# Kernel optimization log

Measured on AMD Instinct MI355X. Metric: run time of the kernel, lower is better.

The kernel has to match this reference:

```python
import jax, jax.numpy as jnp
import numpy as np

NUM_EMBEDDINGS = 8192
EMBEDDING_DIM = 64
COMMITMENT_COST = 0.25


def setup_inputs() -> dict:
    key = jax.random.key(0)
    kx, ke = jax.random.split(key)
    x = jax.random.normal(kx, (32, 1024, EMBEDDING_DIM), dtype=jnp.float32)
    embeddings = jax.random.normal(ke, (NUM_EMBEDDINGS, EMBEDDING_DIM), dtype=jnp.float32)
    return {"x": x, "embeddings": embeddings}


def reference(x, embeddings):
    d = embeddings.shape[1]
    flat_x = x.reshape(-1, d)  # [N, D]
    # squared euclidean distances (argmin identical to cdist argmin):
    d2 = (
        jnp.sum(flat_x * flat_x, axis=-1, keepdims=True)
        - 2.0 * flat_x @ embeddings.T
        + jnp.sum(embeddings * embeddings, axis=-1)
    )
    encoding_indices = jnp.argmin(d2, axis=1)  # [N]
    quantized = embeddings[encoding_indices].reshape(x.shape)
    codebook_loss = jnp.mean((jax.lax.stop_gradient(quantized) - x) ** 2)
    commitment_loss = COMMITMENT_COST * jnp.mean((quantized - jax.lax.stop_gradient(x)) ** 2)
    loss = codebook_loss + commitment_loss
    # straight-through estimator
    quantized_st = x + jax.lax.stop_gradient(quantized - x)
    return quantized_st, loss, encoding_indices
```

## Files before the change

kernel.cpp:

```cpp
#include <hip/hip_runtime.h>
#include <hip/hip_bf16.h>
#include <float.h>

#define N_ROWS 32768
#define DIMS   64
#define K_EMB  8192
#define NT     (K_EMB / 16)
#define NTH    (NT / 2)
#define TSTAGE 8
#define NSTAGE (NTH / TSTAGE)
#define GAP_THR 1.5e-3f

typedef __attribute__((ext_vector_type(8))) short s8v;
typedef __attribute__((ext_vector_type(4))) float f4v;
typedef __attribute__((ext_vector_type(4))) int   i4v;

#define WS_EFRAG 0
#define WS_EN2   (2 * 1024 * 1024)
#define WS_IDX   (WS_EN2 + K_EMB * 4)
#define WS_KEY   (WS_IDX + N_ROWS * 4)
#define WS_BH    (WS_KEY + N_ROWS * 8)
#define WS_SH    (WS_BH + 2 * N_ROWS * 4)
#define WS_CH    (WS_SH + 2 * N_ROWS * 4)
#define WS_CTL   (WS_CH + 2 * N_ROWS * 4)
#define WS_WL    (WS_CTL + 16)

#define OUT_LOSS (N_ROWS * DIMS)
#define OUT_IDX  (N_ROWS * DIMS + 1)

__device__ inline short bfh(float v) {
    __hip_bfloat16 h = __float2bfloat16(v);
    return __builtin_bit_cast(short, h);
}
__device__ inline float bff(short s) {
    __hip_bfloat16 h = __builtin_bit_cast(__hip_bfloat16, s);
    return __bfloat162float(h);
}

__global__ void vq_prep(const float* __restrict__ emb, short* __restrict__ efrag,
                        float* __restrict__ en2) {
    int gid = blockIdx.x * 256 + threadIdx.x;
    int t = gid >> 6, lane = gid & 63;
    int m = lane & 15, q = lane >> 4;
    const float* er = emb + (size_t)(t * 16 + m) * DIMS;
    s8v hi0, lo0, hi1, lo1;
    float ss = 0.f;
#pragma unroll
    for (int j = 0; j < 8; ++j) {
        float v0 = er[q * 8 + j];
        float v1 = er[32 + q * 8 + j];
        ss += v0 * v0 + v1 * v1;
        short h0 = bfh(v0); lo0[j] = bfh(v0 - bff(h0)); hi0[j] = h0;
        short h1 = bfh(v1); lo1[j] = bfh(v1 - bff(h1)); hi1[j] = h1;
    }
    s8v* base = (s8v*)efrag + (size_t)t * 4 * 64;
    base[0 * 64 + lane] = hi0;
    base[1 * 64 + lane] = hi1;
    base[2 * 64 + lane] = lo0;
    base[3 * 64 + lane] = lo1;
    ss += __shfl_xor(ss, 16, 64);
    ss += __shfl_xor(ss, 32, 64);
    if (q == 0) en2[t * 16 + m] = -0.5f * ss;
}

__global__ __launch_bounds__(256, 2) void vq_phase1(
    const float* __restrict__ x, const short* __restrict__ efrag,
    const float* __restrict__ en2,
    float* __restrict__ bh, float* __restrict__ sh, int* __restrict__ ch) {
    __shared__ __align__(16) char lds[2][TSTAGE * 4096];
    int tid = threadIdx.x, wid = tid >> 6, lane = tid & 63;
    int m = lane & 15, q = lane >> 4;
    int kh = blockIdx.y;
    int row0 = blockIdx.x * 128 + wid * 32;

    s8v ahi[2][2], alo[2][2];
#pragma unroll
    for (int g = 0; g < 2; ++g) {
        const float* xr = x + (size_t)(row0 + g * 16 + m) * DIMS + q * 8;
#pragma unroll
        for (int j = 0; j < 8; ++j) {
            float v0 = xr[j], v1 = xr[32 + j];
            short h0 = bfh(v0); alo[g][0][j] = bfh(v0 - bff(h0)); ahi[g][0][j] = h0;
            short h1 = bfh(v1); alo[g][1][j] = bfh(v1 - bff(h1)); ahi[g][1][j] = h1;
        }
    }

    float best[2][4], sec[2][4];
    int bc[2][4];
#pragma unroll
    for (int g = 0; g < 2; ++g)
#pragma unroll
        for (int r = 0; r < 4; ++r) { best[g][r] = -FLT_MAX; sec[g][r] = -FLT_MAX; bc[g][r] = 0; }

    const char* gsrc = (const char*)efrag + (size_t)kh * NTH * 4096;

#pragma unroll
    for (int i = 0; i < 8; ++i)
        __builtin_amdgcn_global_load_lds(
            (const __attribute__((address_space(1))) void*)(gsrc + i * 4096 + tid * 16),
            (__attribute__((address_space(3))) void*)(&lds[0][i * 4096 + tid * 16]),
            16, 0, 0);
    __syncthreads();

    for (int s = 0; s < NSTAGE; ++s) {
        int pb = s & 1;
        if (s + 1 < NSTAGE) {
            const char* gn = gsrc + (size_t)(s + 1) * TSTAGE * 4096;
#pragma unroll
            for (int i = 0; i < 8; ++i)
                __builtin_amdgcn_global_load_lds(
                    (const __attribute__((address_space(1))) void*)(gn + i * 4096 + tid * 16),
                    (__attribute__((address_space(3))) void*)(&lds[pb ^ 1][i * 4096 + tid * 16]),
                    16, 0, 0);
        }
        const i4v* B = (const i4v*)(lds[pb]);
        int tg0 = kh * NTH + s * TSTAGE;
        const float* ep = en2 + (size_t)tg0 * 16 + m;
#pragma unroll
        for (int tt = 0; tt < TSTAGE; ++tt) {
            i4v b0 = B[tt * 256 + 0 * 64 + lane];
            i4v b1 = B[tt * 256 + 1 * 64 + lane];
            i4v b2 = B[tt * 256 + 2 * 64 + lane];
            i4v b3 = B[tt * 256 + 3 * 64 + lane];
            float c0 = ep[tt * 16];
            int cidx = (tg0 + tt) * 16 + m;
#pragma unroll
            for (int g = 0; g < 2; ++g) {
                f4v acc = {c0, c0, c0, c0};
                acc = __builtin_amdgcn_mfma_f32_16x16x32_bf16(ahi[g][0], __builtin_bit_cast(s8v, b0), acc, 0, 0, 0);
                acc = __builtin_amdgcn_mfma_f32_16x16x32_bf16(ahi[g][1], __builtin_bit_cast(s8v, b1), acc, 0, 0, 0);
                acc = __builtin_amdgcn_mfma_f32_16x16x32_bf16(ahi[g][0], __builtin_bit_cast(s8v, b2), acc, 0, 0, 0);
                acc = __builtin_amdgcn_mfma_f32_16x16x32_bf16(ahi[g][1], __builtin_bit_cast(s8v, b3), acc, 0, 0, 0);
                acc = __builtin_amdgcn_mfma_f32_16x16x32_bf16(alo[g][0], __builtin_bit_cast(s8v, b0), acc, 0, 0, 0);
                acc = __builtin_amdgcn_mfma_f32_16x16x32_bf16(alo[g][1], __builtin_bit_cast(s8v, b1), acc, 0, 0, 0);
#pragma unroll
                for (int r = 0; r < 4; ++r) {
                    float v = acc[r];
                    bool gt = v > best[g][r];
                    sec[g][r]  = fmaxf(sec[g][r], fminf(v, best[g][r]));
                    best[g][r] = fmaxf(best[g][r], v);
                    bc[g][r]   = gt ? cidx : bc[g][r];
                }
            }
        }
        __syncthreads();
    }

#pragma unroll
    for (int g = 0; g < 2; ++g)
#pragma unroll
    for (int r = 0; r < 4; ++r) {
        float b = best[g][r], s = sec[g][r];
        int c = bc[g][r];
#pragma unroll
        for (int off = 1; off < 16; off <<= 1) {
            float ob = __shfl_xor(b, off, 64);
            float os = __shfl_xor(s, off, 64);
            int   oc = __shfl_xor(c, off, 64);
            float nb = fmaxf(b, ob);
            float ns = fmaxf(fminf(b, ob), fmaxf(s, os));
            bool take = (ob > b) || (ob == b && oc < c);
            c = take ? oc : c;
            b = nb; s = ns;
        }
        if (m == 0) {
            int o = kh * N_ROWS + row0 + g * 16 + q * 4 + r;
            bh[o] = b; sh[o] = s; ch[o] = c;
        }
    }
}

__global__ void vq_merge(const float* __restrict__ bh, const float* __restrict__ sh,
                         const int* __restrict__ ch, int* __restrict__ idx_buf,
                         unsigned long long* __restrict__ key8,
                         int* __restrict__ wl, int* __restrict__ wl_count) {
    int row = blockIdx.x * 256 + threadIdx.x;
    float b0 = bh[row], b1 = bh[N_ROWS + row];
    float s0 = sh[row], s1 = sh[N_ROWS + row];
    int   c0 = ch[row], c1 = ch[N_ROWS + row];
    float nb = fmaxf(b0, b1);
    float ns = fmaxf(fminf(b0, b1), fmaxf(s0, s1));
    int c = (b1 > b0) ? c1 : c0;
    idx_buf[row] = c;
    key8[row] = 0ULL;
    if (nb - ns < GAP_THR) {
        int pos = atomicAdd(wl_count, 1);
        wl[pos] = row;
    }
}

__global__ __launch_bounds__(256) void vq_fixup(
    const float* __restrict__ x, const float* __restrict__ emb,
    const float* __restrict__ en2, unsigned long long* __restrict__ key8,
    const int* __restrict__ wl, const int* __restrict__ wl_count) {
    __shared__ float4 sx[16];
    __shared__ float sbf[4];
    __shared__ int   sbc[4];
    int tid = threadIdx.x, wid = tid >> 6, lane = tid & 63;
    int cnt = *wl_count;
    for (int wi = blockIdx.x; wi < cnt * 8; wi += gridDim.x) {
        int row = wl[wi >> 3];
        int cbase = (wi & 7) * (K_EMB / 8);
        if (tid < 16) sx[tid] = ((const float4*)(x + (size_t)row * DIMS))[tid];
        __syncthreads();
        float bf_ = -FLT_MAX;
        int bc_ = 0;
        for (int c = cbase + tid; c < cbase + K_EMB / 8; c += 256) {
            const float4* er = (const float4*)(emb + (size_t)c * DIMS);
            float d = 0.f;
#pragma unroll
            for (int qq = 0; qq < 16; ++qq) {
                float4 e = er[qq];
                float4 xx = sx[qq];
                d += e.x * xx.x + e.y * xx.y + e.z * xx.z + e.w * xx.w;
            }
            float f = d + en2[c];
            if (f > bf_) { bf_ = f; bc_ = c; }
        }
#pragma unroll
        for (int off = 1; off < 64; off <<= 1) {
            float of = __shfl_xor(bf_, off, 64);
            int   oc = __shfl_xor(bc_, off, 64);
            if (of > bf_ || (of == bf_ && oc < bc_)) { bf_ = of; bc_ = oc; }
        }
        if (lane == 0) { sbf[wid] = bf_; sbc[wid] = bc_; }
        __syncthreads();
        if (tid == 0) {
            float b = sbf[0]; int c = sbc[0];
#pragma unroll
            for (int i = 1; i < 4; ++i)
                if (sbf[i] > b || (sbf[i] == b && sbc[i] < c)) { b = sbf[i]; c = sbc[i]; }
            unsigned int u = __float_as_uint(b);
            unsigned int sb = ((int)u < 0) ? ~u : (u | 0x80000000u);
            unsigned long long key = ((unsigned long long)sb << 32) | (unsigned int)(~c);
            atomicMax(&key8[row], key);
        }
        __syncthreads();
    }
}

__global__ void vq_gather(const float* __restrict__ x, const float* __restrict__ emb,
                          const int* __restrict__ idx_buf,
                          const unsigned long long* __restrict__ key8,
                          float* __restrict__ out, double* __restrict__ loss_acc) {
    int row = blockIdx.x * blockDim.x + threadIdx.x;
    unsigned long long k = key8[row];
    int idx = k ? (int)(~(unsigned int)k) : idx_buf[row];
    const float4* ev = (const float4*)(emb + (size_t)idx * DIMS);
    const float4* xv = (const float4*)(x + (size_t)row * DIMS);
    float4* ov = (float4*)(out + (size_t)row * DIMS);
    float s = 0.f;
#pragma unroll
    for (int qq = 0; qq < 16; ++qq) {
        float4 ee = ev[qq];
        float4 xx = xv[qq];
        float dx = ee.x - xx.x, dy = ee.y - xx.y, dz = ee.z - xx.z, dw = ee.w - xx.w;
        s += dx * dx + dy * dy + dz * dz + dw * dw;
        ov[qq] = ee;
    }
#pragma unroll
    for (int off = 32; off > 0; off >>= 1) s += __shfl_down(s, off, 64);
    if ((threadIdx.x & 63) == 0) atomicAdd(loss_acc, (double)s);
    out[OUT_IDX + row] = (float)idx;
}

__global__ void vq_loss(const double* __restrict__ acc, float* __restrict__ out) {
    out[OUT_LOSS] = (float)(1.25 * (*acc) / (double)(N_ROWS * DIMS));
}

extern "C" void kernel_launch(void* const* d_in, const int* in_sizes, int n_in,
                              void* d_out, int out_size, void* d_ws, size_t ws_size,
                              hipStream_t stream) {
    const float* x   = (const float*)d_in[0];
    const float* emb = (const float*)d_in[1];
    float* out = (float*)d_out;
    char*  ws  = (char*)d_ws;

    short* efrag   = (short*)(ws + WS_EFRAG);
    float* en2     = (float*)(ws + WS_EN2);
    int*   idx_buf = (int*)(ws + WS_IDX);
    unsigned long long* key8 = (unsigned long long*)(ws + WS_KEY);
    float* bhb     = (float*)(ws + WS_BH);
    float* shb     = (float*)(ws + WS_SH);
    int*   chb     = (int*)(ws + WS_CH);
    double* loss_acc = (double*)(ws + WS_CTL);
    int*   wl_count  = (int*)(ws + WS_CTL + 8);
    int*   wl        = (int*)(ws + WS_WL);

    hipMemsetAsync(ws + WS_CTL, 0, 16, stream);

    vq_prep<<<(NT * 64) / 256, 256, 0, stream>>>(emb, efrag, en2);
    vq_phase1<<<dim3(N_ROWS / 128, 2), 256, 0, stream>>>(x, efrag, en2, bhb, shb, chb);
    vq_merge<<<N_ROWS / 256, 256, 0, stream>>>(bhb, shb, chb, idx_buf, key8, wl, wl_count);
    vq_fixup<<<2048, 256, 0, stream>>>(x, emb, en2, key8, wl, wl_count);
    vq_gather<<<N_ROWS / 256, 256, 0, stream>>>(x, emb, idx_buf, key8, out, loss_acc);
    vq_loss<<<1, 1, 0, stream>>>(loss_acc, out);
}
```

Baseline: 199.6 us.

## Split codebook search into quarters, raise occupancy, restructure fixup as codebook-stationary

```diff
diff --git a/kernel.cpp b/kernel.cpp
--- a/kernel.cpp
+++ b/kernel.cpp
@@ -6,9 +6,10 @@
 #define DIMS   64
 #define K_EMB  8192
 #define NT     (K_EMB / 16)
-#define NTH    (NT / 2)
-#define TSTAGE 8
-#define NSTAGE (NTH / TSTAGE)
+#define NQ     4
+#define NTQ    (NT / NQ)
+#define TSTAGE 4
+#define NSTAGE (NTQ / TSTAGE)
 #define GAP_THR 1.5e-3f
 
 typedef __attribute__((ext_vector_type(8))) short s8v;
@@ -20,9 +21,9 @@
 #define WS_IDX   (WS_EN2 + K_EMB * 4)
 #define WS_KEY   (WS_IDX + N_ROWS * 4)
 #define WS_BH    (WS_KEY + N_ROWS * 8)
-#define WS_SH    (WS_BH + 2 * N_ROWS * 4)
-#define WS_CH    (WS_SH + 2 * N_ROWS * 4)
-#define WS_CTL   (WS_CH + 2 * N_ROWS * 4)
+#define WS_SH    (WS_BH + 4 * N_ROWS * 4)
+#define WS_CH    (WS_SH + 4 * N_ROWS * 4)
+#define WS_CTL   (WS_CH + 4 * N_ROWS * 4)
 #define WS_WL    (WS_CTL + 16)
 
 #define OUT_LOSS (N_ROWS * DIMS)
@@ -63,7 +64,7 @@
     if (q == 0) en2[t * 16 + m] = -0.5f * ss;
 }
 
-__global__ __launch_bounds__(256, 2) void vq_phase1(
+__global__ __launch_bounds__(256, 5) void vq_phase1(
     const float* __restrict__ x, const short* __restrict__ efrag,
     const float* __restrict__ en2,
     float* __restrict__ bh, float* __restrict__ sh, int* __restrict__ ch) {
@@ -92,10 +93,10 @@
 #pragma unroll
         for (int r = 0; r < 4; ++r) { best[g][r] = -FLT_MAX; sec[g][r] = -FLT_MAX; bc[g][r] = 0; }
 
-    const char* gsrc = (const char*)efrag + (size_t)kh * NTH * 4096;
-
-#pragma unroll
-    for (int i = 0; i < 8; ++i)
+    const char* gsrc = (const char*)efrag + (size_t)kh * NTQ * 4096;
+
+#pragma unroll
+    for (int i = 0; i < TSTAGE; ++i)
         __builtin_amdgcn_global_load_lds(
             (const __attribute__((address_space(1))) void*)(gsrc + i * 4096 + tid * 16),
             (__attribute__((address_space(3))) void*)(&lds[0][i * 4096 + tid * 16]),
@@ -107,14 +108,14 @@
         if (s + 1 < NSTAGE) {
             const char* gn = gsrc + (size_t)(s + 1) * TSTAGE * 4096;
 #pragma unroll
-            for (int i = 0; i < 8; ++i)
+            for (int i = 0; i < TSTAGE; ++i)
                 __builtin_amdgcn_global_load_lds(
                     (const __attribute__((address_space(1))) void*)(gn + i * 4096 + tid * 16),
                     (__attribute__((address_space(3))) void*)(&lds[pb ^ 1][i * 4096 + tid * 16]),
                     16, 0, 0);
         }
         const i4v* B = (const i4v*)(lds[pb]);
-        int tg0 = kh * NTH + s * TSTAGE;
+        int tg0 = kh * NTQ + s * TSTAGE;
         const float* ep = en2 + (size_t)tg0 * 16 + m;
 #pragma unroll
         for (int tt = 0; tt < TSTAGE; ++tt) {
@@ -137,7 +138,7 @@
                 for (int r = 0; r < 4; ++r) {
                     float v = acc[r];
                     bool gt = v > best[g][r];
-                    sec[g][r]  = fmaxf(sec[g][r], fminf(v, best[g][r]));
+                    sec[g][r]  = __builtin_amdgcn_fmed3f(v, sec[g][r], best[g][r]);
                     best[g][r] = fmaxf(best[g][r], v);
                     bc[g][r]   = gt ? cidx : bc[g][r];
                 }
@@ -173,69 +174,69 @@
 __global__ void vq_merge(const float* __restrict__ bh, const float* __restrict__ sh,
                          const int* __restrict__ ch, int* __restrict__ idx_buf,
                          unsigned long long* __restrict__ key8,
+                         float* __restrict__ nbv,
                          int* __restrict__ wl, int* __restrict__ wl_count) {
     int row = blockIdx.x * 256 + threadIdx.x;
-    float b0 = bh[row], b1 = bh[N_ROWS + row];
-    float s0 = sh[row], s1 = sh[N_ROWS + row];
-    int   c0 = ch[row], c1 = ch[N_ROWS + row];
-    float nb = fmaxf(b0, b1);
-    float ns = fmaxf(fminf(b0, b1), fmaxf(s0, s1));
-    int c = (b1 > b0) ? c1 : c0;
+    float nb = bh[row];
+    int   c  = ch[row];
+    float ns = -FLT_MAX;
+#pragma unroll
+    for (int h = 1; h < NQ; ++h) {
+        float b = bh[h * N_ROWS + row];
+        int   cc = ch[h * N_ROWS + row];
+        if (b > nb) { ns = nb; nb = b; c = cc; }
+        else        { ns = fmaxf(ns, b); }
+    }
+#pragma unroll
+    for (int h = 0; h < NQ; ++h) ns = fmaxf(ns, sh[h * N_ROWS + row]);
     idx_buf[row] = c;
     key8[row] = 0ULL;
+    nbv[row] = nb;
     if (nb - ns < GAP_THR) {
         int pos = atomicAdd(wl_count, 1);
         wl[pos] = row;
     }
 }
 
-__global__ __launch_bounds__(256) void vq_fixup(
+__global__ __launch_bounds__(64) void vq_fixup(
     const float* __restrict__ x, const float* __restrict__ emb,
-    const float* __restrict__ en2, unsigned long long* __restrict__ key8,
+    const float* __restrict__ en2, const float* __restrict__ nbv,
+    unsigned long long* __restrict__ key8,
     const int* __restrict__ wl, const int* __restrict__ wl_count) {
-    __shared__ float4 sx[16];
-    __shared__ float sbf[4];
-    __shared__ int   sbc[4];
-    int tid = threadIdx.x, wid = tid >> 6, lane = tid & 63;
+    int lane = threadIdx.x;
+    int cchunk = blockIdx.x & 127;
+    int rslice = blockIdx.x >> 7;
+    int c = cchunk * 64 + lane;
+    const float4* er = (const float4*)(emb + (size_t)c * DIMS);
+    float4 e[16];
+#pragma unroll
+    for (int qq = 0; qq < 16; ++qq) e[qq] = er[qq];
+    float c0 = en2[c];
     int cnt = *wl_count;
-    for (int wi = blockIdx.x; wi < cnt * 8; wi += gridDim.x) {
-        int row = wl[wi >> 3];
-        int cbase = (wi & 7) * (K_EMB / 8);
-        if (tid < 16) sx[tid] = ((const float4*)(x + (size_t)row * DIMS))[tid];
-        __syncthreads();
-        float bf_ = -FLT_MAX;
-        int bc_ = 0;
-        for (int c = cbase + tid; c < cbase + K_EMB / 8; c += 256) {
-            const float4* er = (const float4*)(emb + (size_t)c * DIMS);
-            float d = 0.f;
-#pragma unroll
-            for (int qq = 0; qq < 16; ++qq) {
-                float4 e = er[qq];
-                float4 xx = sx[qq];
-                d += e.x * xx.x + e.y * xx.y + e.z * xx.z + e.w * xx.w;
-            }
-            float f = d + en2[c];
-            if (f > bf_) { bf_ = f; bc_ = c; }
-        }
+    for (int wi = rslice; wi < cnt; wi += 16) {
+        int row = wl[wi];
+        const float4* xr = (const float4*)(x + (size_t)row * DIMS);
+        float d = 0.f;
+#pragma unroll
+        for (int qq = 0; qq < 16; ++qq) {
+            float4 ee = e[qq];
+            float4 xx = xr[qq];
+            d += ee.x * xx.x + ee.y * xx.y + ee.z * xx.z + ee.w * xx.w;
+        }
+        float bf_ = d + c0;
+        int bc_ = c;
 #pragma unroll
         for (int off = 1; off < 64; off <<= 1) {
             float of = __shfl_xor(bf_, off, 64);
             int   oc = __shfl_xor(bc_, off, 64);
             if (of > bf_ || (of == bf_ && oc < bc_)) { bf_ = of; bc_ = oc; }
         }
-        if (lane == 0) { sbf[wid] = bf_; sbc[wid] = bc_; }
-        __syncthreads();
-        if (tid == 0) {
-            float b = sbf[0]; int c = sbc[0];
-#pragma unroll
-            for (int i = 1; i < 4; ++i)
-                if (sbf[i] > b || (sbf[i] == b && sbc[i] < c)) { b = sbf[i]; c = sbc[i]; }
-            unsigned int u = __float_as_uint(b);
+        if (lane == 0 && bf_ >= nbv[row] - GAP_THR) {
+            unsigned int u = __float_as_uint(bf_);
             unsigned int sb = ((int)u < 0) ? ~u : (u | 0x80000000u);
-            unsigned long long key = ((unsigned long long)sb << 32) | (unsigned int)(~c);
+            unsigned long long key = ((unsigned long long)sb << 32) | (unsigned int)(~bc_);
             atomicMax(&key8[row], key);
         }
-        __syncthreads();
     }
 }
 
@@ -290,9 +291,9 @@
     hipMemsetAsync(ws + WS_CTL, 0, 16, stream);
 
     vq_prep<<<(NT * 64) / 256, 256, 0, stream>>>(emb, efrag, en2);
-    vq_phase1<<<dim3(N_ROWS / 128, 2), 256, 0, stream>>>(x, efrag, en2, bhb, shb, chb);
-    vq_merge<<<N_ROWS / 256, 256, 0, stream>>>(bhb, shb, chb, idx_buf, key8, wl, wl_count);
-    vq_fixup<<<2048, 256, 0, stream>>>(x, emb, en2, key8, wl, wl_count);
+    vq_phase1<<<dim3(N_ROWS / 128, NQ), 256, 0, stream>>>(x, efrag, en2, bhb, shb, chb);
+    vq_merge<<<N_ROWS / 256, 256, 0, stream>>>(bhb, shb, chb, idx_buf, key8, bhb, wl, wl_count);
+    vq_fixup<<<2048, 64, 0, stream>>>(x, emb, en2, bhb, key8, wl, wl_count);
     vq_gather<<<N_ROWS / 256, 256, 0, stream>>>(x, emb, idx_buf, key8, out, loss_acc);
     vq_loss<<<1, 1, 0, stream>>>(loss_acc, out);
 }
```

Result: slower. 234.2 us (+17.3%).
